# Kernel optimization log

Measured on AMD Instinct MI355X. Metric: run time of the kernel, lower is better.

The kernel has to match this reference:

```python
import jax, jax.numpy as jnp
import numpy as np

EPS = 1e-10

def setup_inputs() -> dict:
    key = jax.random.key(0)
    k1, k2 = jax.random.split(key)
    B, N, D = 8, 4096, 3
    points_ref = jax.random.normal(k1, (B, N, D), dtype=jnp.float32)
    points = jax.random.normal(k2, (B, N, D), dtype=jnp.float32)
    return {"points_ref": points_ref, "points": points, "nn_size": 16}

def _knn(points_ref, K):
    # pairwise squared distances (B,N,N)
    sq = jnp.sum(points_ref * points_ref, axis=-1)
    d2 = sq[:, :, None] + sq[:, None, :] - 2.0 * jnp.einsum('bnd,bmd->bnm', points_ref, points_ref)
    _, idx = jax.lax.top_k(-d2, K)  # nearest first; idx: (B,N,K)
    return idx

def reference(points_ref, points, nn_size):
    K = nn_size + 1
    knn_idx = _knn(points_ref, K)[:, :, 1:]  # drop self -> (B,N,nn_size)
    gather = jax.vmap(lambda p, i: p[i])  # (N,D),(N,K) -> (N,K,D)
    group_ref = gather(points_ref, knn_idx)           # (B,N,K,D)
    group_pred = gather(points, knn_idx)              # (B,N,K,D)
    dist_ref = jnp.linalg.norm(group_ref - points_ref[:, :, None, :], axis=-1)  # (B,N,K)
    dist = jnp.linalg.norm(group_pred - points[:, :, None, :], axis=-1)         # (B,N,K)
    stretch = jnp.maximum(dist / (dist_ref + EPS) - 1.0, 0.0)
    return jnp.mean(stretch)
```

## Files before the change

### kernel.cpp

```cpp
#include <hip/hip_runtime.h>

#define NPTS  4096
#define KNN   16
#define K1    17
#define NBLK  64
#define CELLS 4096
#define EPSF  1e-10f

__device__ __forceinline__ unsigned umin_(unsigned a, unsigned b) { return a < b ? a : b; }
__device__ __forceinline__ unsigned umax_(unsigned a, unsigned b) { return a < b ? b : a; }

#define DPP_XOR1(v)  ((unsigned)__builtin_amdgcn_update_dpp(0, (int)(v), 0xB1, 0xF, 0xF, true))
#define DPP_XOR2(v)  ((unsigned)__builtin_amdgcn_update_dpp(0, (int)(v), 0x4E, 0xF, 0xF, true))
#define SWZ_XOR(v,J) ((unsigned)__builtin_amdgcn_ds_swizzle((int)(v), ((J) << 10) | 0x1F))
#define DPP_SHR1(v)  ((unsigned)__builtin_amdgcn_update_dpp(0, (int)(v), 0x111, 0xF, 0xF, true))
#define DPPF_SHR(vf, CTRL) __uint_as_float((unsigned)__builtin_amdgcn_update_dpp(0, (int)__float_as_uint(vf), CTRL, 0xF, 0xF, true))
#define LXOR1(v)  DPP_XOR1(v)
#define LXOR2(v)  DPP_XOR2(v)
#define LXOR4(v)  SWZ_XOR(v, 4)
#define LXOR8(v)  SWZ_XOR(v, 8)
#define LXOR16(v) SWZ_XOR(v, 16)
#define LXOR32(v) ((unsigned)__shfl_xor((int)(v), 32))

#define BSTEP(K, XORF) do {                                                   \
    unsigned o1_ = XORF(arr), o2_ = XORF(bk);                                 \
    bool tm_ = (((lane & (J_)) == 0) == ((lane & (K)) == 0));                 \
    unsigned mn1_ = umin_(arr, o1_), mx1_ = umax_(arr, o1_);                  \
    unsigned mn2_ = umin_(bk, o2_),  mx2_ = umax_(bk, o2_);                   \
    arr = tm_ ? mn1_ : mx1_; bk = tm_ ? mn2_ : mx2_;                          \
} while (0)

__device__ __forceinline__ unsigned sp4(int v) {
    unsigned x = (unsigned)v;
    return (x & 1u) | ((x & 2u) << 2) | ((x & 4u) << 4) | ((x & 8u) << 6);
}

__global__ __launch_bounds__(1024) void sort_kernel(
    const float* __restrict__ pref,
    float4* __restrict__ wxyzw, int* __restrict__ widx, float4* __restrict__ wbb)
{
    __shared__ unsigned hist[CELLS];
    __shared__ unsigned short cells[NPTS];
    __shared__ unsigned wofs[16];
    const int tid  = threadIdx.x;
    const int lane = tid & 63, w = tid >> 6;
    const int b = blockIdx.x;
    const float* prb = pref + (size_t)b * NPTS * 3;
    const size_t base = (size_t)b * NPTS;

    for (int t = tid; t < CELLS; t += 1024) hist[t] = 0u;
    __syncthreads();

    for (int p = tid; p < NPTS; p += 1024) {
        float x = prb[3 * p + 0], y = prb[3 * p + 1], z = prb[3 * p + 2];
        int cx = min(15, max(0, (int)((x + 4.0f) * 2.0f)));
        int cy = min(15, max(0, (int)((y + 4.0f) * 2.0f)));
        int cz = min(15, max(0, (int)((z + 4.0f) * 2.0f)));
        unsigned m = sp4(cx) | (sp4(cy) << 1) | (sp4(cz) << 2);
        cells[p] = (unsigned short)m;
        atomicAdd(&hist[m], 1u);
    }
    __syncthreads();

    unsigned l0 = hist[4 * tid + 0], l1 = hist[4 * tid + 1];
    unsigned l2 = hist[4 * tid + 2], l3 = hist[4 * tid + 3];
    unsigned s = l0 + l1 + l2 + l3;
    unsigned run = s;
#pragma unroll
    for (int d = 1; d < 64; d <<= 1) {
        unsigned o = __shfl_up(run, d);
        if (lane >= d) run += o;
    }
    if (lane == 63) wofs[w] = run;
    __syncthreads();
    if (tid == 0) {
        unsigned acc = 0;
#pragma unroll
        for (int k = 0; k < 16; ++k) { unsigned t2 = wofs[k]; wofs[k] = acc; acc += t2; }
    }
    __syncthreads();
    unsigned excl = wofs[w] + run - s;
    hist[4 * tid + 0] = excl;
    hist[4 * tid + 1] = excl + l0;
    hist[4 * tid + 2] = excl + l0 + l1;
    hist[4 * tid + 3] = excl + l0 + l1 + l2;
    __syncthreads();

    for (int p = tid; p < NPTS; p += 1024) {
        unsigned c = cells[p];
        unsigned pos = atomicAdd(&hist[c], 1u);
        wxyzw[base + pos] = make_float4(prb[3 * p + 0], prb[3 * p + 1], prb[3 * p + 2], 0.f);
        widx[base + pos]  = p;
    }
    __syncthreads();

#pragma unroll
    for (int rep = 0; rep < 4; ++rep) {
        int blk = w + rep * 16;
        float4 c = wxyzw[base + blk * 64 + lane];
        float mnx = c.x, mxx = c.x, mny = c.y, mxy2 = c.y, mnz = c.z, mxz = c.z;
#pragma unroll
        for (int d = 32; d > 0; d >>= 1) {
            mnx  = fminf(mnx,  __shfl_xor(mnx,  d));
            mxx  = fmaxf(mxx,  __shfl_xor(mxx,  d));
            mny  = fminf(mny,  __shfl_xor(mny,  d));
            mxy2 = fmaxf(mxy2, __shfl_xor(mxy2, d));
            mnz  = fminf(mnz,  __shfl_xor(mnz,  d));
            mxz  = fmaxf(mxz,  __shfl_xor(mxz,  d));
        }
        if (lane == 0) {
            wbb[((size_t)b * NBLK + blk) * 2 + 0] = make_float4(mnx, mny, mnz, 0.f);
            wbb[((size_t)b * NBLK + blk) * 2 + 1] = make_float4(mxx, mxy2, mxz, 0.f);
        }
    }
}

#define EVENTS(KEY) do {                                                      \
    unsigned long long m_ = __ballot((KEY) < thr);                            \
    if (m_) {                                                                 \
        do {                                                                  \
            int l_ = __ffsll(m_) - 1;                                         \
            m_ &= m_ - 1;                                                     \
            unsigned kk_ = (unsigned)__builtin_amdgcn_readlane((int)(KEY), l_);\
            unsigned long long lt_ = __ballot(arr < kk_) & 0x1FFFFull;        \
            int pos_ = __popcll(lt_);                                         \
            unsigned up_ = DPP_SHR1(arr);                                     \
            unsigned a15_ = (unsigned)__builtin_amdgcn_readlane((int)arr, 15);\
            up_ = (lane == 16) ? a15_ : up_;                                  \
            arr = (lane == pos_) ? kk_ : ((lane > pos_) ? up_ : arr);         \
        } while (m_);                                                         \
        thr = (unsigned)__builtin_amdgcn_readlane((int)arr, K1 - 1);          \
    } } while (0)

__global__ __launch_bounds__(128, 8) void knn_main_kernel(
    const float* __restrict__ ppred,
    const float4* __restrict__ wxyzw, const int* __restrict__ widx,
    const float4* __restrict__ wbb, float* __restrict__ partials, int NQ)
{
    const int lane = threadIdx.x & 63;
    const int wv   = blockIdx.x * 2 + (threadIdx.x >> 6);
    const int q = ((NQ & (NQ - 1)) == 0) ? (int)(((unsigned)wv * 26765u) & (unsigned)(NQ - 1)) : wv;

    const int b = q >> 12;
    const int p = q & (NPTS - 1);
    const size_t base = (size_t)b * NPTS;
    const int p0 = p & ~63, ownblk = p >> 6;

    const float4 qc = wxyzw[base + p];
    const float qx = qc.x, qy = qc.y, qz = qc.z;

    unsigned arr;
    {
        float4 c = wxyzw[base + p0 + lane];
        float dx = c.x - qx, dy = c.y - qy, dz = c.z - qz;
        float d2 = dx * dx + dy * dy + dz * dz;
        arr = (__float_as_uint(d2) & 0xFFFFF000u) | (unsigned)(p0 + lane);
    }
    unsigned bk;
    {
        float4 mn4 = wbb[((size_t)b * NBLK + lane) * 2 + 0];
        float4 mx4 = wbb[((size_t)b * NBLK + lane) * 2 + 1];
        float ddx = fmaxf(fmaxf(mn4.x - qx, qx - mx4.x), 0.0f);
        float ddy = fmaxf(fmaxf(mn4.y - qy, qy - mx4.y), 0.0f);
        float ddz = fmaxf(fmaxf(mn4.z - qz, qz - mx4.z), 0.0f);
        float bd2 = ddx * ddx + ddy * ddy + ddz * ddz;
        bk = (__float_as_uint(bd2) & 0xFFFFF000u) | (unsigned)lane;
        bk = (lane == ownblk) ? 0xFFFFFFFFu : bk;
    }

    {
        int J_;
        J_ = 1;  BSTEP(2,  LXOR1);
        J_ = 2;  BSTEP(4,  LXOR2);  J_ = 1; BSTEP(4,  LXOR1);
        J_ = 4;  BSTEP(8,  LXOR4);  J_ = 2; BSTEP(8,  LXOR2);  J_ = 1; BSTEP(8,  LXOR1);
        J_ = 8;  BSTEP(16, LXOR8);  J_ = 4; BSTEP(16, LXOR4);  J_ = 2; BSTEP(16, LXOR2);  J_ = 1; BSTEP(16, LXOR1);
        J_ = 16; BSTEP(32, LXOR16); J_ = 8; BSTEP(32, LXOR8);  J_ = 4; BSTEP(32, LXOR4);  J_ = 2; BSTEP(32, LXOR2); J_ = 1; BSTEP(32, LXOR1);
        J_ = 32; BSTEP(64, LXOR32); J_ = 16; BSTEP(64, LXOR16); J_ = 8; BSTEP(64, LXOR8); J_ = 4; BSTEP(64, LXOR4); J_ = 2; BSTEP(64, LXOR2); J_ = 1; BSTEP(64, LXOR1);
    }
    unsigned thr = (unsigned)__builtin_amdgcn_readlane((int)arr, K1 - 1);

    int k = 0;
    unsigned bcur = (unsigned)__builtin_amdgcn_readlane((int)bk, 0);
    bool have = (bcur < thr);
    float4 cur;
    if (have) cur = wxyzw[base + (int)(bcur & 0xFFFu) * 64 + lane];
    while (have) {
        unsigned bnext = (unsigned)__builtin_amdgcn_readlane((int)bk, k + 1);
        bool pf = (bnext < thr);
        float4 nxt;
        if (pf) nxt = wxyzw[base + (int)(bnext & 0xFFFu) * 64 + lane];
        int jbase = (int)(bcur & 0xFFFu) * 64;
        float dx = cur.x - qx, dy = cur.y - qy, dz = cur.z - qz;
        float d2 = dx * dx + dy * dy + dz * dz;
        unsigned key = (__float_as_uint(d2) & 0xFFFFF000u) | (unsigned)(jbase + lane);
        EVENTS(key);
        ++k;
        bcur = bnext;
        have = (bcur < thr);
        cur = nxt;
    }

    const float* ppb = ppred + (size_t)b * NPTS * 3;
    const int iorig = widx[base + p];
    float s = 0.f;
    if (lane >= 1 && lane <= KNN) {
        int js = (int)(arr & 0xFFFu);
        float4 rc = wxyzw[base + js];
        float rx = rc.x - qx, ry = rc.y - qy, rz = rc.z - qz;
        float dref = sqrtf(rx * rx + ry * ry + rz * rz);
        int nj = widx[base + js];
        float px = ppb[3 * iorig + 0], py = ppb[3 * iorig + 1], pz = ppb[3 * iorig + 2];
        float ax = ppb[3 * nj + 0] - px;
        float ay = ppb[3 * nj + 1] - py;
        float az = ppb[3 * nj + 2] - pz;
        float dpred = sqrtf(ax * ax + ay * ay + az * az);
        s = fmaxf(dpred / (dref + EPSF) - 1.0f, 0.0f);
    }
    s += DPPF_SHR(s, 0x111);
    s += DPPF_SHR(s, 0x112);
    s += DPPF_SHR(s, 0x114);
    s += DPPF_SHR(s, 0x118);
    float t15 = __uint_as_float((unsigned)__builtin_amdgcn_readlane((int)__float_as_uint(s), 15));
    float t16 = __uint_as_float((unsigned)__builtin_amdgcn_readlane((int)__float_as_uint(s), 16));
    if (lane == 0) partials[q] = t15 + t16;
}

__global__ __launch_bounds__(1024) void reduce_kernel(
    const float* __restrict__ partials, int n, float* __restrict__ out, float scale)
{
    __shared__ float wsum[16];
    float s = 0.f;
    for (int idx = threadIdx.x; idx < n; idx += 1024) s += partials[idx];
    for (int off = 32; off > 0; off >>= 1) s += __shfl_down(s, off);
    if ((threadIdx.x & 63) == 0) wsum[threadIdx.x >> 6] = s;
    __syncthreads();
    if (threadIdx.x == 0) {
        float t = 0.f;
#pragma unroll
        for (int k = 0; k < 16; ++k) t += wsum[k];
        out[0] = t * scale;
    }
}

extern "C" void kernel_launch(void* const* d_in, const int* in_sizes, int n_in,
                              void* d_out, int out_size, void* d_ws, size_t ws_size,
                              hipStream_t stream) {
    const float* pref  = (const float*)d_in[0];
    const float* ppred = (const float*)d_in[1];
    float* out = (float*)d_out;

    const int B  = in_sizes[0] / (NPTS * 3);
    const int NQ = B * NPTS;
    const float scale = 1.0f / ((float)NQ * (float)KNN);

    char* ws = (char*)d_ws;
    float4* wxyzw = (float4*)ws;
    int*    widx  = (int*)   (ws + (size_t)B * NPTS * 16);
    float4* wbb   = (float4*)(ws + (size_t)B * NPTS * 20);
    float*  partials = (float*)(ws + (size_t)B * NPTS * 20 + (size_t)B * NBLK * 32);

    sort_kernel<<<dim3(B), dim3(1024), 0, stream>>>(pref, wxyzw, widx, wbb);
    knn_main_kernel<<<dim3(NQ / 2), dim3(128), 0, stream>>>(ppred, wxyzw, widx, wbb, partials, NQ);
    reduce_kernel<<<dim3(1), dim3(1024), 0, stream>>>(partials, NQ, out, scale);
}
```

Measured before the change: 75.52 us.

## Process two queries per wavefront with interleaved bitonic sort and insertion loops

Each wavefront now handles two query points instead of one. Their bitonic sorts, block-scan loops and insertion events are interleaved, and half as many blocks are launched. The aim is more instruction-level parallelism and hidden latency in the long serial readlane, ballot and DPP chains. In exchange, register pressure rises and the two queries' loop trip counts diverge, so one query's work may idle while the other finishes.

```diff
diff --git a/kernel.cpp b/kernel.cpp
--- a/kernel.cpp
+++ b/kernel.cpp
@@ -9,6 +9,9 @@
 
 __device__ __forceinline__ unsigned umin_(unsigned a, unsigned b) { return a < b ? a : b; }
 __device__ __forceinline__ unsigned umax_(unsigned a, unsigned b) { return a < b ? b : a; }
+__device__ __forceinline__ unsigned rdlane(unsigned v, int l) {
+    return (unsigned)__builtin_amdgcn_readlane((int)v, l);
+}
 
 #define DPP_XOR1(v)  ((unsigned)__builtin_amdgcn_update_dpp(0, (int)(v), 0xB1, 0xF, 0xF, true))
 #define DPP_XOR2(v)  ((unsigned)__builtin_amdgcn_update_dpp(0, (int)(v), 0x4E, 0xF, 0xF, true))
@@ -22,12 +25,28 @@
 #define LXOR16(v) SWZ_XOR(v, 16)
 #define LXOR32(v) ((unsigned)__shfl_xor((int)(v), 32))
 
-#define BSTEP(K, XORF) do {                                                   \
-    unsigned o1_ = XORF(arr), o2_ = XORF(bk);                                 \
+#define BSTEP4(K, XORF) do {                                                  \
+    unsigned oa0_ = XORF(arr0), ob0_ = XORF(bk0);                             \
+    unsigned oa1_ = XORF(arr1), ob1_ = XORF(bk1);                             \
     bool tm_ = (((lane & (J_)) == 0) == ((lane & (K)) == 0));                 \
-    unsigned mn1_ = umin_(arr, o1_), mx1_ = umax_(arr, o1_);                  \
-    unsigned mn2_ = umin_(bk, o2_),  mx2_ = umax_(bk, o2_);                   \
-    arr = tm_ ? mn1_ : mx1_; bk = tm_ ? mn2_ : mx2_;                          \
+    unsigned mna0_ = umin_(arr0, oa0_), mxa0_ = umax_(arr0, oa0_);            \
+    unsigned mnb0_ = umin_(bk0,  ob0_), mxb0_ = umax_(bk0,  ob0_);            \
+    unsigned mna1_ = umin_(arr1, oa1_), mxa1_ = umax_(arr1, oa1_);            \
+    unsigned mnb1_ = umin_(bk1,  ob1_), mxb1_ = umax_(bk1,  ob1_);            \
+    arr0 = tm_ ? mna0_ : mxa0_; bk0 = tm_ ? mnb0_ : mxb0_;                    \
+    arr1 = tm_ ? mna1_ : mxa1_; bk1 = tm_ ? mnb1_ : mxb1_;                    \
+} while (0)
+
+#define EV_BODY(KEY, ARR, MM) do {                                            \
+    int l_ = __ffsll(MM) - 1;                                                 \
+    MM &= MM - 1;                                                             \
+    unsigned kk_ = rdlane(KEY, l_);                                           \
+    unsigned long long lt_ = __ballot(ARR < kk_) & 0x1FFFFull;                \
+    int pos_ = __popcll(lt_);                                                 \
+    unsigned up_ = DPP_SHR1(ARR);                                             \
+    unsigned a15_ = rdlane(ARR, 15);                                          \
+    up_ = (lane == 16) ? a15_ : up_;                                          \
+    ARR = (lane == pos_) ? kk_ : ((lane > pos_) ? up_ : ARR);                 \
 } while (0)
 
 __device__ __forceinline__ unsigned sp4(int v) {
@@ -115,23 +134,6 @@
     }
 }
 
-#define EVENTS(KEY) do {                                                      \
-    unsigned long long m_ = __ballot((KEY) < thr);                            \
-    if (m_) {                                                                 \
-        do {                                                                  \
-            int l_ = __ffsll(m_) - 1;                                         \
-            m_ &= m_ - 1;                                                     \
-            unsigned kk_ = (unsigned)__builtin_amdgcn_readlane((int)(KEY), l_);\
-            unsigned long long lt_ = __ballot(arr < kk_) & 0x1FFFFull;        \
-            int pos_ = __popcll(lt_);                                         \
-            unsigned up_ = DPP_SHR1(arr);                                     \
-            unsigned a15_ = (unsigned)__builtin_amdgcn_readlane((int)arr, 15);\
-            up_ = (lane == 16) ? a15_ : up_;                                  \
-            arr = (lane == pos_) ? kk_ : ((lane > pos_) ? up_ : arr);         \
-        } while (m_);                                                         \
-        thr = (unsigned)__builtin_amdgcn_readlane((int)arr, K1 - 1);          \
-    } } while (0)
-
 __global__ __launch_bounds__(128, 8) void knn_main_kernel(
     const float* __restrict__ ppred,
     const float4* __restrict__ wxyzw, const int* __restrict__ widx,
@@ -139,90 +141,163 @@
 {
     const int lane = threadIdx.x & 63;
     const int wv   = blockIdx.x * 2 + (threadIdx.x >> 6);
-    const int q = ((NQ & (NQ - 1)) == 0) ? (int)(((unsigned)wv * 26765u) & (unsigned)(NQ - 1)) : wv;
-
-    const int b = q >> 12;
-    const int p = q & (NPTS - 1);
-    const size_t base = (size_t)b * NPTS;
-    const int p0 = p & ~63, ownblk = p >> 6;
-
-    const float4 qc = wxyzw[base + p];
-    const float qx = qc.x, qy = qc.y, qz = qc.z;
-
-    unsigned arr;
-    {
-        float4 c = wxyzw[base + p0 + lane];
-        float dx = c.x - qx, dy = c.y - qy, dz = c.z - qz;
-        float d2 = dx * dx + dy * dy + dz * dz;
-        arr = (__float_as_uint(d2) & 0xFFFFF000u) | (unsigned)(p0 + lane);
-    }
-    unsigned bk;
-    {
-        float4 mn4 = wbb[((size_t)b * NBLK + lane) * 2 + 0];
-        float4 mx4 = wbb[((size_t)b * NBLK + lane) * 2 + 1];
-        float ddx = fmaxf(fmaxf(mn4.x - qx, qx - mx4.x), 0.0f);
-        float ddy = fmaxf(fmaxf(mn4.y - qy, qy - mx4.y), 0.0f);
-        float ddz = fmaxf(fmaxf(mn4.z - qz, qz - mx4.z), 0.0f);
-        float bd2 = ddx * ddx + ddy * ddy + ddz * ddz;
-        bk = (__float_as_uint(bd2) & 0xFFFFF000u) | (unsigned)lane;
-        bk = (lane == ownblk) ? 0xFFFFFFFFu : bk;
+    const bool pow2 = (NQ & (NQ - 1)) == 0;
+    const int qid0 = wv * 2, qid1 = wv * 2 + 1;
+    const int q0 = pow2 ? (int)(((unsigned)qid0 * 26765u) & (unsigned)(NQ - 1)) : qid0;
+    const int q1 = pow2 ? (int)(((unsigned)qid1 * 26765u) & (unsigned)(NQ - 1)) : qid1;
+
+    const int b0 = q0 >> 12, b1 = q1 >> 12;
+    const int p0 = q0 & (NPTS - 1), p1 = q1 & (NPTS - 1);
+    const size_t base0 = (size_t)b0 * NPTS, base1 = (size_t)b1 * NPTS;
+    const int pb0 = p0 & ~63, pb1 = p1 & ~63;
+    const int ownblk0 = p0 >> 6, ownblk1 = p1 >> 6;
+
+    const float4 qc0 = wxyzw[base0 + p0];
+    const float4 qc1 = wxyzw[base1 + p1];
+    const float qx0 = qc0.x, qy0 = qc0.y, qz0 = qc0.z;
+    const float qx1 = qc1.x, qy1 = qc1.y, qz1 = qc1.z;
+
+    unsigned arr0, arr1;
+    {
+        float4 c0 = wxyzw[base0 + pb0 + lane];
+        float4 c1 = wxyzw[base1 + pb1 + lane];
+        float dx0 = c0.x - qx0, dy0 = c0.y - qy0, dz0 = c0.z - qz0;
+        float dx1 = c1.x - qx1, dy1 = c1.y - qy1, dz1 = c1.z - qz1;
+        float d20 = dx0 * dx0 + dy0 * dy0 + dz0 * dz0;
+        float d21 = dx1 * dx1 + dy1 * dy1 + dz1 * dz1;
+        arr0 = (__float_as_uint(d20) & 0xFFFFF000u) | (unsigned)(pb0 + lane);
+        arr1 = (__float_as_uint(d21) & 0xFFFFF000u) | (unsigned)(pb1 + lane);
+    }
+    unsigned bk0, bk1;
+    {
+        float4 mn0 = wbb[((size_t)b0 * NBLK + lane) * 2 + 0];
+        float4 mx0 = wbb[((size_t)b0 * NBLK + lane) * 2 + 1];
+        float4 mn1 = wbb[((size_t)b1 * NBLK + lane) * 2 + 0];
+        float4 mx1 = wbb[((size_t)b1 * NBLK + lane) * 2 + 1];
+        float dx0 = fmaxf(fmaxf(mn0.x - qx0, qx0 - mx0.x), 0.0f);
+        float dy0 = fmaxf(fmaxf(mn0.y - qy0, qy0 - mx0.y), 0.0f);
+        float dz0 = fmaxf(fmaxf(mn0.z - qz0, qz0 - mx0.z), 0.0f);
+        float dx1 = fmaxf(fmaxf(mn1.x - qx1, qx1 - mx1.x), 0.0f);
+        float dy1 = fmaxf(fmaxf(mn1.y - qy1, qy1 - mx1.y), 0.0f);
+        float dz1 = fmaxf(fmaxf(mn1.z - qz1, qz1 - mx1.z), 0.0f);
+        float bd0 = dx0 * dx0 + dy0 * dy0 + dz0 * dz0;
+        float bd1 = dx1 * dx1 + dy1 * dy1 + dz1 * dz1;
+        bk0 = (__float_as_uint(bd0) & 0xFFFFF000u) | (unsigned)lane;
+        bk1 = (__float_as_uint(bd1) & 0xFFFFF000u) | (unsigned)lane;
+        bk0 = (lane == ownblk0) ? 0xFFFFFFFFu : bk0;
+        bk1 = (lane == ownblk1) ? 0xFFFFFFFFu : bk1;
     }
 
     {
         int J_;
-        J_ = 1;  BSTEP(2,  LXOR1);
-        J_ = 2;  BSTEP(4,  LXOR2);  J_ = 1; BSTEP(4,  LXOR1);
-        J_ = 4;  BSTEP(8,  LXOR4);  J_ = 2; BSTEP(8,  LXOR2);  J_ = 1; BSTEP(8,  LXOR1);
-        J_ = 8;  BSTEP(16, LXOR8);  J_ = 4; BSTEP(16, LXOR4);  J_ = 2; BSTEP(16, LXOR2);  J_ = 1; BSTEP(16, LXOR1);
-        J_ = 16; BSTEP(32, LXOR16); J_ = 8; BSTEP(32, LXOR8);  J_ = 4; BSTEP(32, LXOR4);  J_ = 2; BSTEP(32, LXOR2); J_ = 1; BSTEP(32, LXOR1);
-        J_ = 32; BSTEP(64, LXOR32); J_ = 16; BSTEP(64, LXOR16); J_ = 8; BSTEP(64, LXOR8); J_ = 4; BSTEP(64, LXOR4); J_ = 2; BSTEP(64, LXOR2); J_ = 1; BSTEP(64, LXOR1);
-    }
-    unsigned thr = (unsigned)__builtin_amdgcn_readlane((int)arr, K1 - 1);
-
-    int k = 0;
-    unsigned bcur = (unsigned)__builtin_amdgcn_readlane((int)bk, 0);
-    bool have = (bcur < thr);
-    float4 cur;
-    if (have) cur = wxyzw[base + (int)(bcur & 0xFFFu) * 64 + lane];
-    while (have) {
-        unsigned bnext = (unsigned)__builtin_amdgcn_readlane((int)bk, k + 1);
-        bool pf = (bnext < thr);
-        float4 nxt;
-        if (pf) nxt = wxyzw[base + (int)(bnext & 0xFFFu) * 64 + lane];
-        int jbase = (int)(bcur & 0xFFFu) * 64;
-        float dx = cur.x - qx, dy = cur.y - qy, dz = cur.z - qz;
-        float d2 = dx * dx + dy * dy + dz * dz;
-        unsigned key = (__float_as_uint(d2) & 0xFFFFF000u) | (unsigned)(jbase + lane);
-        EVENTS(key);
-        ++k;
-        bcur = bnext;
-        have = (bcur < thr);
-        cur = nxt;
-    }
-
-    const float* ppb = ppred + (size_t)b * NPTS * 3;
-    const int iorig = widx[base + p];
-    float s = 0.f;
-    if (lane >= 1 && lane <= KNN) {
-        int js = (int)(arr & 0xFFFu);
-        float4 rc = wxyzw[base + js];
-        float rx = rc.x - qx, ry = rc.y - qy, rz = rc.z - qz;
-        float dref = sqrtf(rx * rx + ry * ry + rz * rz);
-        int nj = widx[base + js];
-        float px = ppb[3 * iorig + 0], py = ppb[3 * iorig + 1], pz = ppb[3 * iorig + 2];
-        float ax = ppb[3 * nj + 0] - px;
-        float ay = ppb[3 * nj + 1] - py;
-        float az = ppb[3 * nj + 2] - pz;
-        float dpred = sqrtf(ax * ax + ay * ay + az * az);
-        s = fmaxf(dpred / (dref + EPSF) - 1.0f, 0.0f);
-    }
-    s += DPPF_SHR(s, 0x111);
-    s += DPPF_SHR(s, 0x112);
-    s += DPPF_SHR(s, 0x114);
-    s += DPPF_SHR(s, 0x118);
-    float t15 = __uint_as_float((unsigned)__builtin_amdgcn_readlane((int)__float_as_uint(s), 15));
-    float t16 = __uint_as_float((unsigned)__builtin_amdgcn_readlane((int)__float_as_uint(s), 16));
-    if (lane == 0) partials[q] = t15 + t16;
+        J_ = 1;  BSTEP4(2,  LXOR1);
+        J_ = 2;  BSTEP4(4,  LXOR2);  J_ = 1; BSTEP4(4,  LXOR1);
+        J_ = 4;  BSTEP4(8,  LXOR4);  J_ = 2; BSTEP4(8,  LXOR2);  J_ = 1; BSTEP4(8,  LXOR1);
+        J_ = 8;  BSTEP4(16, LXOR8);  J_ = 4; BSTEP4(16, LXOR4);  J_ = 2; BSTEP4(16, LXOR2);  J_ = 1; BSTEP4(16, LXOR1);
+        J_ = 16; BSTEP4(32, LXOR16); J_ = 8; BSTEP4(32, LXOR8);  J_ = 4; BSTEP4(32, LXOR4);  J_ = 2; BSTEP4(32, LXOR2); J_ = 1; BSTEP4(32, LXOR1);
+        J_ = 32; BSTEP4(64, LXOR32); J_ = 16; BSTEP4(64, LXOR16); J_ = 8; BSTEP4(64, LXOR8); J_ = 4; BSTEP4(64, LXOR4); J_ = 2; BSTEP4(64, LXOR2); J_ = 1; BSTEP4(64, LXOR1);
+    }
+    unsigned thr0 = rdlane(arr0, K1 - 1);
+    unsigned thr1 = rdlane(arr1, K1 - 1);
+
+    int k0 = 0, k1 = 0;
+    unsigned bcur0 = rdlane(bk0, 0), bcur1 = rdlane(bk1, 0);
+    bool have0 = (bcur0 < thr0), have1 = (bcur1 < thr1);
+    float4 cur0, cur1;
+    if (have0) cur0 = wxyzw[base0 + (int)(bcur0 & 0xFFFu) * 64 + lane];
+    if (have1) cur1 = wxyzw[base1 + (int)(bcur1 & 0xFFFu) * 64 + lane];
+
+    while (have0 || have1) {
+        unsigned long long m0 = 0, m1 = 0;
+        unsigned key0 = 0, key1 = 0, bnext0 = 0, bnext1 = 0;
+        float4 nxt0, nxt1;
+        bool pf0 = false, pf1 = false;
+        if (have0) {
+            bnext0 = rdlane(bk0, k0 + 1);
+            pf0 = (bnext0 < thr0);
+            if (pf0) nxt0 = wxyzw[base0 + (int)(bnext0 & 0xFFFu) * 64 + lane];
+            float dx = cur0.x - qx0, dy = cur0.y - qy0, dz = cur0.z - qz0;
+            float d2 = dx * dx + dy * dy + dz * dz;
+            key0 = (__float_as_uint(d2) & 0xFFFFF000u) | (unsigned)((int)(bcur0 & 0xFFFu) * 64 + lane);
+            m0 = __ballot(key0 < thr0);
+        }
+        if (have1) {
+            bnext1 = rdlane(bk1, k1 + 1);
+            pf1 = (bnext1 < thr1);
+            if (pf1) nxt1 = wxyzw[base1 + (int)(bnext1 & 0xFFFu) * 64 + lane];
+            float dx = cur1.x - qx1, dy = cur1.y - qy1, dz = cur1.z - qz1;
+            float d2 = dx * dx + dy * dy + dz * dz;
+            key1 = (__float_as_uint(d2) & 0xFFFFF000u) | (unsigned)((int)(bcur1 & 0xFFFu) * 64 + lane);
+            m1 = __ballot(key1 < thr1);
+        }
+        while (m0 | m1) {
+            if (m0) EV_BODY(key0, arr0, m0);
+            if (m1) EV_BODY(key1, arr1, m1);
+        }
+        if (have0) {
+            thr0 = rdlane(arr0, K1 - 1);
+            ++k0; bcur0 = bnext0;
+            have0 = (bcur0 < thr0);
+            cur0 = nxt0;
+        }
+        if (have1) {
+            thr1 = rdlane(arr1, K1 - 1);
+            ++k1; bcur1 = bnext1;
+            have1 = (bcur1 < thr1);
+            cur1 = nxt1;
+        }
+    }
+
+    {
+        const float* ppb = ppred + (size_t)b0 * NPTS * 3;
+        const int iorig = widx[base0 + p0];
+        float s = 0.f;
+        if (lane >= 1 && lane <= KNN) {
+            int js = (int)(arr0 & 0xFFFu);
+            float4 rc = wxyzw[base0 + js];
+            float rx = rc.x - qx0, ry = rc.y - qy0, rz = rc.z - qz0;
+            float dref = sqrtf(rx * rx + ry * ry + rz * rz);
+            int nj = widx[base0 + js];
+            float px = ppb[3 * iorig + 0], py = ppb[3 * iorig + 1], pz = ppb[3 * iorig + 2];
+            float ax = ppb[3 * nj + 0] - px;
+            float ay = ppb[3 * nj + 1] - py;
+            float az = ppb[3 * nj + 2] - pz;
+            float dpred = sqrtf(ax * ax + ay * ay + az * az);
+            s = fmaxf(dpred / (dref + EPSF) - 1.0f, 0.0f);
+        }
+        s += DPPF_SHR(s, 0x111);
+        s += DPPF_SHR(s, 0x112);
+        s += DPPF_SHR(s, 0x114);
+        s += DPPF_SHR(s, 0x118);
+        float t15 = __uint_as_float(rdlane(__float_as_uint(s), 15));
+        float t16 = __uint_as_float(rdlane(__float_as_uint(s), 16));
+        if (lane == 0) partials[q0] = t15 + t16;
+    }
+    {
+        const float* ppb = ppred + (size_t)b1 * NPTS * 3;
+        const int iorig = widx[base1 + p1];
+        float s = 0.f;
+        if (lane >= 1 && lane <= KNN) {
+            int js = (int)(arr1 & 0xFFFu);
+            float4 rc = wxyzw[base1 + js];
+            float rx = rc.x - qx1, ry = rc.y - qy1, rz = rc.z - qz1;
+            float dref = sqrtf(rx * rx + ry * ry + rz * rz);
+            int nj = widx[base1 + js];
+            float px = ppb[3 * iorig + 0], py = ppb[3 * iorig + 1], pz = ppb[3 * iorig + 2];
+            float ax = ppb[3 * nj + 0] - px;
+            float ay = ppb[3 * nj + 1] - py;
+            float az = ppb[3 * nj + 2] - pz;
+            float dpred = sqrtf(ax * ax + ay * ay + az * az);
+            s = fmaxf(dpred / (dref + EPSF) - 1.0f, 0.0f);
+        }
+        s += DPPF_SHR(s, 0x111);
+        s += DPPF_SHR(s, 0x112);
+        s += DPPF_SHR(s, 0x114);
+        s += DPPF_SHR(s, 0x118);
+        float t15 = __uint_as_float(rdlane(__float_as_uint(s), 15));
+        float t16 = __uint_as_float(rdlane(__float_as_uint(s), 16));
+        if (lane == 0) partials[q1] = t15 + t16;
+    }
 }
 
 __global__ __launch_bounds__(1024) void reduce_kernel(
@@ -260,6 +335,6 @@
     float*  partials = (float*)(ws + (size_t)B * NPTS * 20 + (size_t)B * NBLK * 32);
 
     sort_kernel<<<dim3(B), dim3(1024), 0, stream>>>(pref, wxyzw, widx, wbb);
-    knn_main_kernel<<<dim3(NQ / 2), dim3(128), 0, stream>>>(ppred, wxyzw, widx, wbb, partials, NQ);
+    knn_main_kernel<<<dim3(NQ / 4), dim3(128), 0, stream>>>(ppred, wxyzw, widx, wbb, partials, NQ);
     reduce_kernel<<<dim3(1), dim3(1024), 0, stream>>>(partials, NQ, out, scale);
 }
```

Result: slower. 84.28 us (+11.6%).

## Group sixteen consecutive query waves per 1024-thread block

Applied to the files above, without the earlier changes.

The main kNN kernel now launches 1024-thread blocks, each holding 16 waves that handle 16 consecutive queries of a scrambled group. Before, each 2-wave block handled two scattered queries. Spatially neighbouring queries in the same block should touch the same candidate blocks, which may improve cache locality and cut block launch overhead. The trade-offs are a looser launch bound, which may raise register use, and coarser scheduling that could worsen load imbalance from the variable-length candidate loop.

```diff
diff --git a/kernel.cpp b/kernel.cpp
--- a/kernel.cpp
+++ b/kernel.cpp
@@ -5,10 +5,14 @@
 #define K1    17
 #define NBLK  64
 #define CELLS 4096
+#define WPB   16
 #define EPSF  1e-10f
 
 __device__ __forceinline__ unsigned umin_(unsigned a, unsigned b) { return a < b ? a : b; }
 __device__ __forceinline__ unsigned umax_(unsigned a, unsigned b) { return a < b ? b : a; }
+__device__ __forceinline__ unsigned rdlane(unsigned v, int l) {
+    return (unsigned)__builtin_amdgcn_readlane((int)v, l);
+}
 
 #define DPP_XOR1(v)  ((unsigned)__builtin_amdgcn_update_dpp(0, (int)(v), 0xB1, 0xF, 0xF, true))
 #define DPP_XOR2(v)  ((unsigned)__builtin_amdgcn_update_dpp(0, (int)(v), 0x4E, 0xF, 0xF, true))
@@ -121,25 +125,29 @@
         do {                                                                  \
             int l_ = __ffsll(m_) - 1;                                         \
             m_ &= m_ - 1;                                                     \
-            unsigned kk_ = (unsigned)__builtin_amdgcn_readlane((int)(KEY), l_);\
+            unsigned kk_ = rdlane(KEY, l_);                                   \
             unsigned long long lt_ = __ballot(arr < kk_) & 0x1FFFFull;        \
             int pos_ = __popcll(lt_);                                         \
             unsigned up_ = DPP_SHR1(arr);                                     \
-            unsigned a15_ = (unsigned)__builtin_amdgcn_readlane((int)arr, 15);\
+            unsigned a15_ = rdlane(arr, 15);                                  \
             up_ = (lane == 16) ? a15_ : up_;                                  \
             arr = (lane == pos_) ? kk_ : ((lane > pos_) ? up_ : arr);         \
         } while (m_);                                                         \
-        thr = (unsigned)__builtin_amdgcn_readlane((int)arr, K1 - 1);          \
+        thr = rdlane(arr, K1 - 1);                                            \
     } } while (0)
 
-__global__ __launch_bounds__(128, 8) void knn_main_kernel(
+__global__ __launch_bounds__(1024) void knn_main_kernel(
     const float* __restrict__ ppred,
     const float4* __restrict__ wxyzw, const int* __restrict__ widx,
     const float4* __restrict__ wbb, float* __restrict__ partials, int NQ)
 {
     const int lane = threadIdx.x & 63;
-    const int wv   = blockIdx.x * 2 + (threadIdx.x >> 6);
-    const int q = ((NQ & (NQ - 1)) == 0) ? (int)(((unsigned)wv * 26765u) & (unsigned)(NQ - 1)) : wv;
+    const int w    = threadIdx.x >> 6;
+    const int ngrp = NQ / WPB;
+    const int g = ((ngrp & (ngrp - 1)) == 0)
+                ? (int)(((unsigned)blockIdx.x * 26765u) & (unsigned)(ngrp - 1))
+                : blockIdx.x;
+    const int q = g * WPB + w;
 
     const int b = q >> 12;
     const int p = q & (NPTS - 1);
@@ -177,15 +185,15 @@
         J_ = 16; BSTEP(32, LXOR16); J_ = 8; BSTEP(32, LXOR8);  J_ = 4; BSTEP(32, LXOR4);  J_ = 2; BSTEP(32, LXOR2); J_ = 1; BSTEP(32, LXOR1);
         J_ = 32; BSTEP(64, LXOR32); J_ = 16; BSTEP(64, LXOR16); J_ = 8; BSTEP(64, LXOR8); J_ = 4; BSTEP(64, LXOR4); J_ = 2; BSTEP(64, LXOR2); J_ = 1; BSTEP(64, LXOR1);
     }
-    unsigned thr = (unsigned)__builtin_amdgcn_readlane((int)arr, K1 - 1);
+    unsigned thr = rdlane(arr, K1 - 1);
 
     int k = 0;
-    unsigned bcur = (unsigned)__builtin_amdgcn_readlane((int)bk, 0);
+    unsigned bcur = rdlane(bk, 0);
     bool have = (bcur < thr);
     float4 cur;
     if (have) cur = wxyzw[base + (int)(bcur & 0xFFFu) * 64 + lane];
     while (have) {
-        unsigned bnext = (unsigned)__builtin_amdgcn_readlane((int)bk, k + 1);
+        unsigned bnext = rdlane(bk, k + 1);
         bool pf = (bnext < thr);
         float4 nxt;
         if (pf) nxt = wxyzw[base + (int)(bnext & 0xFFFu) * 64 + lane];
@@ -220,8 +228,8 @@
     s += DPPF_SHR(s, 0x112);
     s += DPPF_SHR(s, 0x114);
     s += DPPF_SHR(s, 0x118);
-    float t15 = __uint_as_float((unsigned)__builtin_amdgcn_readlane((int)__float_as_uint(s), 15));
-    float t16 = __uint_as_float((unsigned)__builtin_amdgcn_readlane((int)__float_as_uint(s), 16));
+    float t15 = __uint_as_float(rdlane(__float_as_uint(s), 15));
+    float t16 = __uint_as_float(rdlane(__float_as_uint(s), 16));
     if (lane == 0) partials[q] = t15 + t16;
 }
 
@@ -260,6 +268,6 @@
     float*  partials = (float*)(ws + (size_t)B * NPTS * 20 + (size_t)B * NBLK * 32);
 
     sort_kernel<<<dim3(B), dim3(1024), 0, stream>>>(pref, wxyzw, widx, wbb);
-    knn_main_kernel<<<dim3(NQ / 2), dim3(128), 0, stream>>>(ppred, wxyzw, widx, wbb, partials, NQ);
+    knn_main_kernel<<<dim3(NQ / WPB), dim3(1024), 0, stream>>>(ppred, wxyzw, widx, wbb, partials, NQ);
     reduce_kernel<<<dim3(1), dim3(1024), 0, stream>>>(partials, NQ, out, scale);
 }
```

Measured after the change: 80.23 us. +6.2%, slower.
